# Optimization experiments

Hardware: AMD Instinct MI355X
Metric: run time of the kernel (lower is better)

The kernel has to match this reference:

```python
import jax, jax.numpy as jnp
import numpy as np

D_PRIME = 512
D = 2048
CLASSES = 4


def setup_inputs() -> dict:
    key = jax.random.key(0)
    k1, k2, k3, k4 = jax.random.split(key, 4)
    N = 32768
    V_prime = jax.random.normal(k1, (N, D), dtype=jnp.float32)
    U_t = jax.random.normal(k2, (D_PRIME, D), dtype=jnp.float32)
    W_mta = jax.random.normal(k3, (1, D_PRIME), dtype=jnp.float32)
    W = jax.random.normal(k4, (CLASSES, D), dtype=jnp.float32)
    return {"V_prime": V_prime, "U_t": U_t, "W_mta": W_mta, "W": W}


def reference(V_prime, U_t, W_mta, W):
    # [D_prime, N] = tanh(U_t @ V'^T)
    tanh_scores = jnp.tanh(U_t @ V_prime.T)
    # attention over instances: [1, N]
    a = jax.nn.softmax(W_mta @ tanh_scores, axis=1)
    # weighted sum pooling: [D]
    t = jnp.sum(a.T * V_prime, axis=0)
    # final linear: [1, classes]
    l = (W @ t).reshape(1, CLASSES)
    return l
```

## Files before the change

### kernel.cpp

```cpp
#include <hip/hip_runtime.h>

#define N_INST 32768
#define DIM    2048
#define DP     512
#define NCLS   4

typedef _Float16 half8_t  __attribute__((ext_vector_type(8)));
typedef float    float4_t __attribute__((ext_vector_type(4)));

#define OFF_UHI   0ull
#define OFF_S     (OFF_UHI  + (size_t)DP*DIM*2)
#define OFF_STAT  (OFF_S    + (size_t)N_INST*4)
#define OFF_PSTAT (OFF_STAT + 256ull)
#define OFF_T     (OFF_PSTAT+ 256ull)

__device__ __forceinline__ float tanh_fast(float x) {
  float e = __expf(2.0f * x);
  return 1.0f - 2.0f / (e + 1.0f);
}

typedef const unsigned int __attribute__((address_space(1)))* gas_t;
typedef unsigned int       __attribute__((address_space(3)))* las_t;
__device__ __forceinline__ void gl16(const void* g, void* l) {
  __builtin_amdgcn_global_load_lds((gas_t)g, (las_t)l, 16, 0, 0);
}

__global__ __launch_bounds__(256) void k_cvt(const float4* __restrict__ in,
                                             half8_t* __restrict__ out) {
  int i = blockIdx.x * 256 + threadIdx.x;
  float4 a = in[2 * i], b = in[2 * i + 1];
  half8_t h;
  h[0] = (_Float16)a.x; h[1] = (_Float16)a.y;
  h[2] = (_Float16)a.z; h[3] = (_Float16)a.w;
  h[4] = (_Float16)b.x; h[5] = (_Float16)b.y;
  h[6] = (_Float16)b.z; h[7] = (_Float16)b.w;
  out[i] = h;
}

__global__ __launch_bounds__(256) void k_score_gemm(
    const _Float16* __restrict__ Uhi, const float* __restrict__ V,
    const float* __restrict__ Wmta, float* __restrict__ s) {
  __shared__ _Float16 lA[128 * 32];
  __shared__ float    lB[128 * 32];

  const int tid  = threadIdx.x;
  const int lane = tid & 63;
  const int wv   = tid >> 6;
  const int waveM = wv >> 1;
  const int waveN = wv & 1;
  const int quad = lane >> 4;
  const int col  = lane & 15;

  const int b   = blockIdx.x;
  const int grp = b >> 5;
  const int win = b & 31;
  const int mb  = win >> 3;
  const int nb  = grp * 8 + (win & 7);

  const int aRow0  = mb * 128;
  const int bRow0  = nb * 128;
  const int kStart = (nb & 63) << 5;

  const int rA0 = wv * 32 + (lane >> 2);
  const int sA  = (lane & 3) ^ ((rA0 >> 1) & 3);
  const _Float16* gA0 = Uhi + (size_t)(aRow0 + rA0) * DIM + sA * 8;
  const _Float16* gA1 = gA0 + (size_t)16 * DIM;
  _Float16* lAd0 = &lA[(wv * 2 + 0) * 512];
  _Float16* lAd1 = &lA[(wv * 2 + 1) * 512];

  const int rB0 = wv * 32 + (lane >> 3);
  const int sB  = (lane & 7) ^ (rB0 & 7);
  const float* gB0 = V + (size_t)(bRow0 + rB0) * DIM + sB * 4;
  const float* gB1 = gB0 + (size_t)8  * DIM;
  const float* gB2 = gB0 + (size_t)16 * DIM;
  const float* gB3 = gB0 + (size_t)24 * DIM;
  float* lBd0 = &lB[(wv * 4 + 0) * 256];
  float* lBd1 = &lB[(wv * 4 + 1) * 256];
  float* lBd2 = &lB[(wv * 4 + 2) * 256];
  float* lBd3 = &lB[(wv * 4 + 3) * 256];

  int offA[4];
#pragma unroll
  for (int mi = 0; mi < 4; ++mi) {
    const int r = waveM * 64 + mi * 16 + col;
    offA[mi] = r * 64 + ((quad ^ ((r >> 1) & 3)) << 4);
  }
  int offB[4];
#pragma unroll
  for (int ni = 0; ni < 4; ++ni) {
    const int r = waveN * 64 + ni * 16 + col;
    offB[ni] = r * 128 + ((((quad << 1)) ^ (r & 7)) << 4);
  }

  float4_t acc[4][4];
  const float4_t z4 = {0.f, 0.f, 0.f, 0.f};
#pragma unroll
  for (int i = 0; i < 4; i++)
#pragma unroll
    for (int j = 0; j < 4; j++) acc[i][j] = z4;

  const char* lAc = (const char*)lA;
  const char* lBc = (const char*)lB;

  for (int ki = 0; ki < 64; ++ki) {
    const int k = (kStart + (ki << 5)) & (DIM - 1);
    __syncthreads();
    gl16(gA0 + k, lAd0);
    gl16(gA1 + k, lAd1);
    gl16(gB0 + k, lBd0);
    gl16(gB1 + k, lBd1);
    gl16(gB2 + k, lBd2);
    gl16(gB3 + k, lBd3);
    __syncthreads();

    half8_t af[4];
#pragma unroll
    for (int mi = 0; mi < 4; ++mi)
      af[mi] = *(const half8_t*)(lAc + offA[mi]);

#pragma unroll
    for (int ni = 0; ni < 4; ++ni) {
      const float4_t x = *(const float4_t*)(lBc + offB[ni]);
      const float4_t y = *(const float4_t*)(lBc + (offB[ni] ^ 16));
      const auto c0 = __builtin_amdgcn_cvt_pkrtz(x[0], x[1]);
      const auto c1 = __builtin_amdgcn_cvt_pkrtz(x[2], x[3]);
      const auto c2 = __builtin_amdgcn_cvt_pkrtz(y[0], y[1]);
      const auto c3 = __builtin_amdgcn_cvt_pkrtz(y[2], y[3]);
      half8_t bf;
      bf[0] = (_Float16)c0[0]; bf[1] = (_Float16)c0[1];
      bf[2] = (_Float16)c1[0]; bf[3] = (_Float16)c1[1];
      bf[4] = (_Float16)c2[0]; bf[5] = (_Float16)c2[1];
      bf[6] = (_Float16)c3[0]; bf[7] = (_Float16)c3[1];
#pragma unroll
      for (int mi = 0; mi < 4; ++mi)
        acc[mi][ni] = __builtin_amdgcn_mfma_f32_16x16x32_f16(af[mi], bf, acc[mi][ni], 0, 0, 0);
    }
  }

#pragma unroll
  for (int ni = 0; ni < 4; ni++) {
    float v = 0.0f;
#pragma unroll
    for (int mi = 0; mi < 4; mi++) {
      const int jb = aRow0 + waveM * 64 + mi * 16 + quad * 4;
      union { float4_t v4; float f[4]; } u;
      u.v4 = acc[mi][ni];
#pragma unroll
      for (int r = 0; r < 4; r++)
        v += Wmta[jb + r] * tanh_fast(u.f[r]);
    }
    v += __shfl_xor(v, 16);
    v += __shfl_xor(v, 32);
    if (quad == 0) {
      const int n = bRow0 + waveN * 64 + ni * 16 + col;
      atomicAdd(&s[n], v);
    }
  }
}

__global__ __launch_bounds__(256) void k_stats1(const float* __restrict__ s,
                                                float* __restrict__ pstat) {
  const int tid = threadIdx.x;
  const int lane = tid & 63;
  const int wvi = tid >> 6;
  __shared__ float smM[4], smP[4];
  const float4* s4 = (const float4*)s;

  float4 v = s4[blockIdx.x * 256 + tid];
  float m = fmaxf(fmaxf(v.x, v.y), fmaxf(v.z, v.w));
  float p = __expf(v.x - m) + __expf(v.y - m) + __expf(v.z - m) + __expf(v.w - m);
  for (int o = 32; o > 0; o >>= 1) {
    float om = __shfl_xor(m, o);
    float op = __shfl_xor(p, o);
    float nm = fmaxf(m, om);
    p = p * __expf(m - nm) + op * __expf(om - nm);
    m = nm;
  }
  if (lane == 0) { smM[wvi] = m; smP[wvi] = p; }
  __syncthreads();
  if (tid == 0) {
    float gm = fmaxf(fmaxf(smM[0], smM[1]), fmaxf(smM[2], smM[3]));
    float sum = 0.f;
    for (int w = 0; w < 4; w++) sum += smP[w] * __expf(smM[w] - gm);
    pstat[blockIdx.x * 2]     = gm;
    pstat[blockIdx.x * 2 + 1] = sum;
  }
}

__global__ __launch_bounds__(64) void k_stats2(const float* __restrict__ pstat,
                                               float* __restrict__ stats) {
  const int tid = threadIdx.x;
  float m = -3.4e38f, p = 0.0f;
  if (tid < 32) { m = pstat[tid * 2]; p = pstat[tid * 2 + 1]; }
  for (int o = 32; o > 0; o >>= 1) {
    float om = __shfl_xor(m, o);
    float op = __shfl_xor(p, o);
    float nm = fmaxf(m, om);
    p = p * __expf(m - nm) + op * __expf(om - nm);
    m = nm;
  }
  if (tid == 0) { stats[0] = m; stats[1] = 1.0f / p; }
}

__global__ __launch_bounds__(256) void k_pool(const float* __restrict__ V,
                                              const float* __restrict__ s,
                                              const float* __restrict__ stats,
                                              float* __restrict__ t) {
  __shared__ float wsm[128];
  __shared__ int hot;
  const int tid = threadIdx.x;
  if (tid == 0) hot = 0;
  __syncthreads();
  const float mx = stats[0], inv = stats[1];
  const int n0 = blockIdx.x * 128;
  if (tid < 128) {
    const float w = __expf(s[n0 + tid] - mx) * inv;
    wsm[tid] = w;
    if (w > 1e-12f) atomicOr(&hot, 1);
  }
  __syncthreads();
  if (hot == 0) return;

  float acc[8] = {0.f, 0.f, 0.f, 0.f, 0.f, 0.f, 0.f, 0.f};
  for (int r = 0; r < 128; ++r) {
    const float w = wsm[r];
    if (w > 1e-12f) {
      const float4* vp = (const float4*)&V[(size_t)(n0 + r) * DIM + tid * 8];
      float4 va = vp[0], vb = vp[1];
      acc[0] += w * va.x; acc[1] += w * va.y; acc[2] += w * va.z; acc[3] += w * va.w;
      acc[4] += w * vb.x; acc[5] += w * vb.y; acc[6] += w * vb.z; acc[7] += w * vb.w;
    }
  }
#pragma unroll
  for (int j = 0; j < 8; ++j) atomicAdd(&t[tid * 8 + j], acc[j]);
}

__global__ __launch_bounds__(256) void k_final(const float* __restrict__ t,
                                               const float* __restrict__ W,
                                               float* __restrict__ out) {
  const int tid = threadIdx.x;
  const float4* t4 = (const float4*)t;
  const float4 ta = t4[tid * 2], tb = t4[tid * 2 + 1];
  float pc[NCLS];
#pragma unroll
  for (int c = 0; c < NCLS; ++c) {
    const float4* w4 = (const float4*)&W[(size_t)c * DIM + tid * 8];
    const float4 wa = w4[0], wb = w4[1];
    pc[c] = wa.x * ta.x + wa.y * ta.y + wa.z * ta.z + wa.w * ta.w +
            wb.x * tb.x + wb.y * tb.y + wb.z * tb.z + wb.w * tb.w;
  }
  __shared__ float sred[4][NCLS];
  const int lane = tid & 63, wvi = tid >> 6;
#pragma unroll
  for (int c = 0; c < NCLS; ++c)
    for (int o = 32; o > 0; o >>= 1) pc[c] += __shfl_xor(pc[c], o);
  if (lane == 0)
#pragma unroll
    for (int c = 0; c < NCLS; ++c) sred[wvi][c] = pc[c];
  __syncthreads();
  if (tid < NCLS)
    out[tid] = sred[0][tid] + sred[1][tid] + sred[2][tid] + sred[3][tid];
}

extern "C" void kernel_launch(void* const* d_in, const int* in_sizes, int n_in,
                              void* d_out, int out_size, void* d_ws, size_t ws_size,
                              hipStream_t stream) {
  const float* Vp   = (const float*)d_in[0];
  const float* Ut   = (const float*)d_in[1];
  const float* Wmta = (const float*)d_in[2];
  const float* W    = (const float*)d_in[3];
  float* out = (float*)d_out;

  char* ws = (char*)d_ws;
  _Float16* Uhi  = (_Float16*)(ws + OFF_UHI);
  float*    sBuf = (float*)(ws + OFF_S);
  float*    stat = (float*)(ws + OFF_STAT);
  float*    pstat= (float*)(ws + OFF_PSTAT);
  float*    tvec = (float*)(ws + OFF_T);

  hipMemsetAsync(sBuf, 0, (size_t)N_INST * 4, stream);
  hipMemsetAsync(tvec, 0, (size_t)DIM * 4, stream);

  k_cvt<<<(DP * DIM / 8) / 256, 256, 0, stream>>>((const float4*)Ut, (half8_t*)Uhi);
  k_score_gemm<<<(DP / 128) * (N_INST / 128), 256, 0, stream>>>(Uhi, Vp, Wmta, sBuf);
  k_stats1<<<32, 256, 0, stream>>>(sBuf, pstat);
  k_stats2<<<1, 64, 0, stream>>>(pstat, stat);
  k_pool<<<N_INST / 128, 256, 0, stream>>>(Vp, sBuf, stat, tvec);
  k_final<<<1, 256, 0, stream>>>(tvec, W, out);
}
```

Before: 537.4 us.

## Double-buffer LDS tiles in score GEMM to overlap loads with MFMA

```diff
diff --git a/kernel.cpp b/kernel.cpp
--- a/kernel.cpp
+++ b/kernel.cpp
@@ -40,8 +40,8 @@
 __global__ __launch_bounds__(256) void k_score_gemm(
     const _Float16* __restrict__ Uhi, const float* __restrict__ V,
     const float* __restrict__ Wmta, float* __restrict__ s) {
-  __shared__ _Float16 lA[128 * 32];
-  __shared__ float    lB[128 * 32];
+  __shared__ _Float16 lA[2][128 * 32];
+  __shared__ float    lB[2][128 * 32];
 
   const int tid  = threadIdx.x;
   const int lane = tid & 63;
@@ -65,8 +65,8 @@
   const int sA  = (lane & 3) ^ ((rA0 >> 1) & 3);
   const _Float16* gA0 = Uhi + (size_t)(aRow0 + rA0) * DIM + sA * 8;
   const _Float16* gA1 = gA0 + (size_t)16 * DIM;
-  _Float16* lAd0 = &lA[(wv * 2 + 0) * 512];
-  _Float16* lAd1 = &lA[(wv * 2 + 1) * 512];
+  const int dA0 = (wv * 2 + 0) * 512;
+  const int dA1 = (wv * 2 + 1) * 512;
 
   const int rB0 = wv * 32 + (lane >> 3);
   const int sB  = (lane & 7) ^ (rB0 & 7);
@@ -74,10 +74,10 @@
   const float* gB1 = gB0 + (size_t)8  * DIM;
   const float* gB2 = gB0 + (size_t)16 * DIM;
   const float* gB3 = gB0 + (size_t)24 * DIM;
-  float* lBd0 = &lB[(wv * 4 + 0) * 256];
-  float* lBd1 = &lB[(wv * 4 + 1) * 256];
-  float* lBd2 = &lB[(wv * 4 + 2) * 256];
-  float* lBd3 = &lB[(wv * 4 + 3) * 256];
+  const int dB0 = (wv * 4 + 0) * 256;
+  const int dB1 = (wv * 4 + 1) * 256;
+  const int dB2 = (wv * 4 + 2) * 256;
+  const int dB3 = (wv * 4 + 3) * 256;
 
   int offA[4];
 #pragma unroll
@@ -99,43 +99,56 @@
 #pragma unroll
     for (int j = 0; j < 4; j++) acc[i][j] = z4;
 
-  const char* lAc = (const char*)lA;
-  const char* lBc = (const char*)lB;
-
-  for (int ki = 0; ki < 64; ++ki) {
-    const int k = (kStart + (ki << 5)) & (DIM - 1);
+#define STAGE(buf, k) do {                       \
+    gl16(gA0 + (k), &lA[buf][dA0]);              \
+    gl16(gA1 + (k), &lA[buf][dA1]);              \
+    gl16(gB0 + (k), &lB[buf][dB0]);              \
+    gl16(gB1 + (k), &lB[buf][dB1]);              \
+    gl16(gB2 + (k), &lB[buf][dB2]);              \
+    gl16(gB3 + (k), &lB[buf][dB3]);              \
+  } while (0)
+
+#define COMPUTE(buf) do {                                                  \
+    const char* lAc = (const char*)&lA[buf][0];                            \
+    const char* lBc = (const char*)&lB[buf][0];                            \
+    half8_t af[4];                                                         \
+    _Pragma("unroll")                                                      \
+    for (int mi = 0; mi < 4; ++mi)                                         \
+      af[mi] = *(const half8_t*)(lAc + offA[mi]);                          \
+    _Pragma("unroll")                                                      \
+    for (int ni = 0; ni < 4; ++ni) {                                       \
+      const float4_t x = *(const float4_t*)(lBc + offB[ni]);               \
+      const float4_t y = *(const float4_t*)(lBc + (offB[ni] ^ 16));        \
+      const auto c0 = __builtin_amdgcn_cvt_pkrtz(x[0], x[1]);              \
+      const auto c1 = __builtin_amdgcn_cvt_pkrtz(x[2], x[3]);              \
+      const auto c2 = __builtin_amdgcn_cvt_pkrtz(y[0], y[1]);              \
+      const auto c3 = __builtin_amdgcn_cvt_pkrtz(y[2], y[3]);              \
+      half8_t bf;                                                          \
+      bf[0] = (_Float16)c0[0]; bf[1] = (_Float16)c0[1];                    \
+      bf[2] = (_Float16)c1[0]; bf[3] = (_Float16)c1[1];                    \
+      bf[4] = (_Float16)c2[0]; bf[5] = (_Float16)c2[1];                    \
+      bf[6] = (_Float16)c3[0]; bf[7] = (_Float16)c3[1];                    \
+      _Pragma("unroll")                                                    \
+      for (int mi = 0; mi < 4; ++mi)                                       \
+        acc[mi][ni] = __builtin_amdgcn_mfma_f32_16x16x32_f16(              \
+            af[mi], bf, acc[mi][ni], 0, 0, 0);                             \
+    }                                                                      \
+  } while (0)
+
+  STAGE(0, kStart);
+
+  for (int kk = 0; kk < 32; ++kk) {
+    const int kB = (kStart + (2 * kk + 1) * 32) & (DIM - 1);
+    const int kC = (kStart + (2 * kk + 2) * 32) & (DIM - 1);
     __syncthreads();
-    gl16(gA0 + k, lAd0);
-    gl16(gA1 + k, lAd1);
-    gl16(gB0 + k, lBd0);
-    gl16(gB1 + k, lBd1);
-    gl16(gB2 + k, lBd2);
-    gl16(gB3 + k, lBd3);
+    STAGE(1, kB);
+    COMPUTE(0);
     __syncthreads();
-
-    half8_t af[4];
-#pragma unroll
-    for (int mi = 0; mi < 4; ++mi)
-      af[mi] = *(const half8_t*)(lAc + offA[mi]);
-
-#pragma unroll
-    for (int ni = 0; ni < 4; ++ni) {
-      const float4_t x = *(const float4_t*)(lBc + offB[ni]);
-      const float4_t y = *(const float4_t*)(lBc + (offB[ni] ^ 16));
-      const auto c0 = __builtin_amdgcn_cvt_pkrtz(x[0], x[1]);
-      const auto c1 = __builtin_amdgcn_cvt_pkrtz(x[2], x[3]);
-      const auto c2 = __builtin_amdgcn_cvt_pkrtz(y[0], y[1]);
-      const auto c3 = __builtin_amdgcn_cvt_pkrtz(y[2], y[3]);
-      half8_t bf;
-      bf[0] = (_Float16)c0[0]; bf[1] = (_Float16)c0[1];
-      bf[2] = (_Float16)c1[0]; bf[3] = (_Float16)c1[1];
-      bf[4] = (_Float16)c2[0]; bf[5] = (_Float16)c2[1];
-      bf[6] = (_Float16)c3[0]; bf[7] = (_Float16)c3[1];
-#pragma unroll
-      for (int mi = 0; mi < 4; ++mi)
-        acc[mi][ni] = __builtin_amdgcn_mfma_f32_16x16x32_f16(af[mi], bf, acc[mi][ni], 0, 0, 0);
-    }
-  }
+    if (kk < 31) STAGE(0, kC);
+    COMPUTE(1);
+  }
+#undef STAGE
+#undef COMPUTE
 
 #pragma unroll
   for (int ni = 0; ni < 4; ni++) {
```

Result: faster. 507.8 us (-5.5%).
